# Performance work log

Hardware: AMD Instinct MI355X
Metric: run time of the kernel (lower is better)

Reference implementation:

```python
import jax, jax.numpy as jnp
import numpy as np
from jax import lax

OC = 128
KH, KW = 2, 2


def setup_inputs() -> dict:
    key = jax.random.key(0)
    k1, k2, k3 = jax.random.split(key, 3)
    C = 256
    n = C * KH * KW
    stdv = 1.0 / np.sqrt(n)
    x = jax.random.normal(k1, (16, C, 64, 64), dtype=jnp.float32)
    # original allocates (oc^2*kh*kw, C, kh, kw) but only uses first oc*kh*kw rows
    weight = jax.random.uniform(k2, (OC * OC * KH * KW, C, KH, KW), dtype=jnp.float32,
                                minval=-stdv, maxval=stdv)
    bias = jax.random.uniform(k3, (OC * (KH + KW),), dtype=jnp.float32,
                              minval=-stdv, maxval=stdv)
    return {"x": x, "weight": weight, "bias": bias}


def _robin_shuffle(x, weight, bias):
    # output[b,z,p,q] = stride-1 valid conv at (p,q) using filter
    # index (p%KH)*KW + (q%KW) + z*KH*KW, plus matching bias.
    nf = OC * KH * KW
    w = weight[:nf]  # (nf, C, KH, KW)
    full = lax.conv_general_dilated(
        x, w, window_strides=(1, 1), padding='VALID',
        dimension_numbers=('NCHW', 'OIHW', 'NCHW'))  # (N, nf, H', W')
    full = full + bias[:nf][None, :, None, None]
    N, _, Hp, Wp = full.shape
    full = full.reshape(N, OC, KH * KW, Hp, Wp)
    idx = (jnp.arange(Hp)[:, None] % KH) * KW + (jnp.arange(Wp)[None, :] % KW)  # (H', W')
    out = jnp.take_along_axis(full, idx[None, None, None, :, :], axis=2)
    return out.squeeze(2)  # (N, OC, H', W')


def reference(x, weight, bias):
    return _robin_shuffle(x, weight, bias)
```

## Files before the change

kernel.cpp:

```cpp
#include <hip/hip_runtime.h>

typedef __bf16 v8bf __attribute__((ext_vector_type(8)));
typedef float f32x4 __attribute__((ext_vector_type(4)));
typedef unsigned int u32;

#define C_IN 256
#define HW   64
#define OHW  63
#define NOC  128

__global__ void wprep(const float* __restrict__ w, __bf16* __restrict__ Wf) {
  int f = blockIdx.x;
  int c = threadIdx.x;
  f32x4 v = *(const f32x4*)(w + (size_t)f * 1024 + c * 4);
  int oc = f >> 2, kp = f & 3;
#pragma unroll
  for (int khkw = 0; khkw < 4; ++khkw)
    Wf[(((size_t)(kp * 4 + khkw) * 32 + (c >> 3)) * 128 + oc) * 8 + (c & 7)] =
        (__bf16)v[khkw];
}

__global__ __launch_bounds__(1024, 4) void robin_main(
    const float* __restrict__ x, const __bf16* __restrict__ Wf,
    const float* __restrict__ bias, float* __restrict__ out) {
  __shared__ __align__(16) char smem[42240];
  char* xb0 = smem;
  char* xb1 = smem + 21120;

  const int tid  = threadIdx.x;
  const int lane = tid & 63;
  const int wid  = tid >> 6;
  const int hb   = blockIdx.x;
  const int n    = blockIdx.y;
  const int h0   = hb * 4;

  const int ocg  = wid >> 2;
  const int kp   = wid & 3;
  const int ph   = kp >> 1, pw = kp & 1;
  const int lcol = lane & 15;
  const int lg   = lane >> 4;

  if (tid < 80) {
    int g  = tid & 7;
    int t2 = tid >> 3;
    int dy = t2 % 5, bi = t2 / 5;
    f32x4 z = {0.f, 0.f, 0.f, 0.f};
    *(f32x4*)((bi ? xb1 : xb0) + (dy * 33 + 32) * 128 + g * 16) = z;
  }

  int boff[4];
#pragma unroll
  for (int khkw = 0; khkw < 4; ++khkw) {
    int kh = khkw >> 1, kw = khkw & 1;
    int dy0  = ph + kh;
    int wcol = 2 * lcol + pw + kw;
    int wp_  = wcol >> 1;
    boff[khkw] = ((dy0 * 33 + wp_) * 128 + (wcol & 1) * 64 + lg * 16) ^
                 ((wp_ & 7) << 4);
  }

  f32x4 acc[2][4];
#pragma unroll
  for (int m = 0; m < 2; ++m)
#pragma unroll
    for (int f = 0; f < 4; ++f) acc[m][f] = (f32x4){0.f, 0.f, 0.f, 0.f};

  const float* xbase = x + (size_t)n * C_IN * HW * HW;

  const int wp_s  = lane >> 1;
  const int par_s = lane & 1;
  const int bo_s  = ((wp_s * 128) + par_s * 64 + wid * 4) ^ ((wp_s & 7) << 4);
  float xlo[5], xhi[5];
  v8bf  a_reg[4][2];

#define A_LOAD(QQ)                                                             \
  {                                                                            \
    _Pragma("unroll") for (int khkw = 0; khkw < 4; ++khkw) {                   \
      const __bf16* wp =                                                       \
          Wf + (((size_t)(kp * 4 + khkw) * 32 + (QQ) * 4 + lg) * 128 +        \
                ocg * 32 + lcol) * 8;                                          \
      a_reg[khkw][0] = *(const v8bf*)wp;                                       \
      a_reg[khkw][1] = *(const v8bf*)(wp + 128);                               \
    }                                                                          \
  }

#define LOADQ(QQ)                                                              \
  {                                                                            \
    const float* bp =                                                          \
        xbase + ((size_t)((QQ) * 32 + 2 * wid)) * 4096 + h0 * 64 + lane;       \
    _Pragma("unroll") for (int k = 0; k < 4; ++k) {                            \
      xlo[k] = bp[k * 64];                                                     \
      xhi[k] = bp[4096 + k * 64];                                              \
    }                                                                          \
    if (h0 + 4 < HW) {                                                         \
      xlo[4] = bp[4 * 64];                                                     \
      xhi[4] = bp[4096 + 4 * 64];                                              \
    } else {                                                                   \
      xlo[4] = 0.f;                                                            \
      xhi[4] = 0.f;                                                            \
    }                                                                          \
  }

#define WRITEQ(QQ)                                                             \
  {                                                                            \
    char* xd = ((QQ) & 1) ? xb1 : xb0;                                         \
    _Pragma("unroll") for (int k = 0; k < 5; ++k) {                            \
      unsigned short a_ = __builtin_bit_cast(unsigned short, (__bf16)xlo[k]);  \
      unsigned short b_ = __builtin_bit_cast(unsigned short, (__bf16)xhi[k]);  \
      *(u32*)(xd + bo_s + k * 4224) = (u32)a_ | ((u32)b_ << 16);               \
    }                                                                          \
  }

#define COMPUTE(QQ)                                                            \
  {                                                                            \
    const char* xsb = ((QQ) & 1) ? xb1 : xb0;                                  \
    _Pragma("unroll") for (int khkw = 0; khkw < 4; ++khkw) {                   \
      v8bf b[4];                                                               \
      _Pragma("unroll") for (int r = 0; r < 2; ++r)                            \
        _Pragma("unroll") for (int hh = 0; hh < 2; ++hh)                       \
          b[r * 2 + hh] =                                                      \
              *(const v8bf*)(xsb + boff[khkw] + r * 8448 + hh * 2048);         \
      _Pragma("unroll") for (int m = 0; m < 2; ++m)                            \
        _Pragma("unroll") for (int f = 0; f < 4; ++f)                          \
          acc[m][f] = __builtin_amdgcn_mfma_f32_16x16x32_bf16(                 \
              a_reg[khkw][m], b[f], acc[m][f], 0, 0, 0);                       \
    }                                                                          \
  }

  LOADQ(0);
  WRITEQ(0);
  __syncthreads();

  for (int q = 0; q < 8; ++q) {
    A_LOAD(q);
    if (q < 7) LOADQ(q + 1);
    COMPUTE(q);
    if (q < 7) {
      WRITEQ(q + 1);
      __syncthreads();
    }
  }

  float bv[2][4];
#pragma unroll
  for (int m = 0; m < 2; ++m)
#pragma unroll
    for (int reg = 0; reg < 4; ++reg)
      bv[m][reg] = bias[(ocg * 32 + m * 16 + lg * 4 + reg) * 4 + kp];

  float* eb = (float*)smem;
#pragma unroll
  for (int p = 0; p < 4; ++p) {
    const int h = h0 + p;
    __syncthreads();
    if ((ph == (p & 1)) && h < OHW) {
      const int rsel = p >> 1;
#pragma unroll
      for (int m = 0; m < 2; ++m)
#pragma unroll
        for (int hh = 0; hh < 2; ++hh) {
          f32x4 v = acc[m][rsel * 2 + hh];
          int w = 2 * (hh * 16 + lcol) + pw;
#pragma unroll
          for (int reg = 0; reg < 4; ++reg)
            eb[(ocg * 32 + m * 16 + lg * 4 + reg) * 68 + w] =
                v[reg] + bv[m][reg];
        }
    }
    __syncthreads();
    if (h < OHW) {
      const int lc2 = tid & 15;
#pragma unroll
      for (int s = 0; s < 2; ++s) {
        int oc = (tid >> 4) + (s << 6);
        float* orow = out + ((size_t)(n * NOC + oc) * OHW + h) * OHW;
        const float* erow = eb + oc * 68;
#pragma unroll
        for (int b = 0; b < 4; ++b) {
          int w = lc2 + 16 * b;
          if (w < OHW) orow[w] = erow[w];
        }
      }
    }
  }
#undef A_LOAD
#undef LOADQ
#undef WRITEQ
#undef COMPUTE
}

extern "C" void kernel_launch(void* const* d_in, const int* in_sizes, int n_in,
                              void* d_out, int out_size, void* d_ws, size_t ws_size,
                              hipStream_t stream) {
  const float* x      = (const float*)d_in[0];
  const float* weight = (const float*)d_in[1];
  const float* bias   = (const float*)d_in[2];
  float* out          = (float*)d_out;
  __bf16* Wf          = (__bf16*)d_ws;

  wprep<<<512, 256, 0, stream>>>(weight, Wf);
  robin_main<<<dim3(16, 16), 1024, 0, stream>>>(x, Wf, bias, out);
}
```

Measured before the change: 42.92 us.

## Quad-buffer LDS input tiles and sync once per two channel chunks

Raises the shared-memory input staging from two buffers to four and keeps two register sets of prefetched x values. The main loop now handles two channel chunks per iteration with a single barrier, and global loads are issued further ahead of the compute that uses them. The goal is fewer __syncthreads and better hiding of global-load latency. In exchange, LDS use doubles to about 84KB per block and register pressure rises under 1024-thread launch bounds, which can reduce occupancy or cause spills.

```diff
diff --git a/kernel.cpp b/kernel.cpp
--- a/kernel.cpp
+++ b/kernel.cpp
@@ -8,6 +8,7 @@
 #define HW   64
 #define OHW  63
 #define NOC  128
+#define BUFSZ 21120
 
 __global__ void wprep(const float* __restrict__ w, __bf16* __restrict__ Wf) {
   int f = blockIdx.x;
@@ -23,9 +24,7 @@
 __global__ __launch_bounds__(1024, 4) void robin_main(
     const float* __restrict__ x, const __bf16* __restrict__ Wf,
     const float* __restrict__ bias, float* __restrict__ out) {
-  __shared__ __align__(16) char smem[42240];
-  char* xb0 = smem;
-  char* xb1 = smem + 21120;
+  __shared__ __align__(16) char smem[4 * BUFSZ];
 
   const int tid  = threadIdx.x;
   const int lane = tid & 63;
@@ -40,12 +39,12 @@
   const int lcol = lane & 15;
   const int lg   = lane >> 4;
 
-  if (tid < 80) {
+  if (tid < 160) {
     int g  = tid & 7;
     int t2 = tid >> 3;
     int dy = t2 % 5, bi = t2 / 5;
     f32x4 z = {0.f, 0.f, 0.f, 0.f};
-    *(f32x4*)((bi ? xb1 : xb0) + (dy * 33 + 32) * 128 + g * 16) = z;
+    *(f32x4*)(smem + bi * BUFSZ + (dy * 33 + 32) * 128 + g * 16) = z;
   }
 
   int boff[4];
@@ -70,7 +69,7 @@
   const int wp_s  = lane >> 1;
   const int par_s = lane & 1;
   const int bo_s  = ((wp_s * 128) + par_s * 64 + wid * 4) ^ ((wp_s & 7) << 4);
-  float xlo[5], xhi[5];
+  float xloA[5], xhiA[5], xloB[5], xhiB[5];
   v8bf  a_reg[4][2];
 
 #define A_LOAD(QQ)                                                             \
@@ -84,36 +83,36 @@
     }                                                                          \
   }
 
-#define LOADQ(QQ)                                                              \
+#define LOADQ(QQ, XLO, XHI)                                                    \
   {                                                                            \
     const float* bp =                                                          \
         xbase + ((size_t)((QQ) * 32 + 2 * wid)) * 4096 + h0 * 64 + lane;       \
     _Pragma("unroll") for (int k = 0; k < 4; ++k) {                            \
-      xlo[k] = bp[k * 64];                                                     \
-      xhi[k] = bp[4096 + k * 64];                                              \
+      XLO[k] = bp[k * 64];                                                     \
+      XHI[k] = bp[4096 + k * 64];                                              \
     }                                                                          \
     if (h0 + 4 < HW) {                                                         \
-      xlo[4] = bp[4 * 64];                                                     \
-      xhi[4] = bp[4096 + 4 * 64];                                              \
+      XLO[4] = bp[4 * 64];                                                     \
+      XHI[4] = bp[4096 + 4 * 64];                                              \
     } else {                                                                   \
-      xlo[4] = 0.f;                                                            \
-      xhi[4] = 0.f;                                                            \
-    }                                                                          \
-  }
-
-#define WRITEQ(QQ)                                                             \
-  {                                                                            \
-    char* xd = ((QQ) & 1) ? xb1 : xb0;                                         \
+      XLO[4] = 0.f;                                                            \
+      XHI[4] = 0.f;                                                            \
+    }                                                                          \
+  }
+
+#define WRITEQ(QQ, XLO, XHI)                                                   \
+  {                                                                            \
+    char* xd = smem + ((QQ) & 3) * BUFSZ;                                      \
     _Pragma("unroll") for (int k = 0; k < 5; ++k) {                            \
-      unsigned short a_ = __builtin_bit_cast(unsigned short, (__bf16)xlo[k]);  \
-      unsigned short b_ = __builtin_bit_cast(unsigned short, (__bf16)xhi[k]);  \
+      unsigned short a_ = __builtin_bit_cast(unsigned short, (__bf16)XLO[k]);  \
+      unsigned short b_ = __builtin_bit_cast(unsigned short, (__bf16)XHI[k]);  \
       *(u32*)(xd + bo_s + k * 4224) = (u32)a_ | ((u32)b_ << 16);               \
     }                                                                          \
   }
 
 #define COMPUTE(QQ)                                                            \
   {                                                                            \
-    const char* xsb = ((QQ) & 1) ? xb1 : xb0;                                  \
+    const char* xsb = smem + ((QQ) & 3) * BUFSZ;                               \
     _Pragma("unroll") for (int khkw = 0; khkw < 4; ++khkw) {                   \
       v8bf b[4];                                                               \
       _Pragma("unroll") for (int r = 0; r < 2; ++r)                            \
@@ -127,19 +126,29 @@
     }                                                                          \
   }
 
-  LOADQ(0);
-  WRITEQ(0);
+  LOADQ(0, xloA, xhiA);
+  WRITEQ(0, xloA, xhiA);
+  LOADQ(1, xloB, xhiB);
+  WRITEQ(1, xloB, xhiB);
+  LOADQ(2, xloA, xhiA);
   __syncthreads();
 
-  for (int q = 0; q < 8; ++q) {
-    A_LOAD(q);
-    if (q < 7) LOADQ(q + 1);
-    COMPUTE(q);
-    if (q < 7) {
-      WRITEQ(q + 1);
-      __syncthreads();
-    }
-  }
+  for (int p = 0; p < 3; ++p) {
+    const int q0 = 2 * p;
+    A_LOAD(q0);
+    WRITEQ(q0 + 2, xloA, xhiA);
+    LOADQ(q0 + 3, xloB, xhiB);
+    COMPUTE(q0);
+    A_LOAD(q0 + 1);
+    WRITEQ(q0 + 3, xloB, xhiB);
+    if (p < 2) LOADQ(q0 + 4, xloA, xhiA);
+    COMPUTE(q0 + 1);
+    __syncthreads();
+  }
+  A_LOAD(6);
+  COMPUTE(6);
+  A_LOAD(7);
+  COMPUTE(7);
 
   float bv[2][4];
 #pragma unroll
```

New measurement: 42.07 us. -2.0%, faster.
